# Optimization experiments

Measured on AMD Instinct MI355X. Metric: run time of the kernel, lower is better.

The kernel has to match this reference:

```python
import jax, jax.numpy as jnp
import numpy as np

# Mex config (matches init_kwargs)
B, C, H, W = 64, 64, 64, 64
BLK = (64, 3, 3)        # block over (C, H, W); spans all channels -> out_c = 1
STR = (64, 2, 2)
PAD = (0, 1, 1)
NI = 256                # num_instances
EPS = 1.0
SOFTMAX_MODE = False    # False -> mean (logsumexp - log k), True -> plain logsumexp


def setup_inputs() -> dict:
    key = jax.random.key(0)
    k1, k2 = jax.random.split(key)
    x = jax.random.normal(k1, (B, C, H, W), dtype=jnp.float32)
    kblk = BLK[0] * BLK[1] * BLK[2]
    # Dirichlet([1]*k) init == normalized exponentials; nregions = 1 (shared offsets)
    e = jax.random.exponential(k2, (1, NI, kblk), dtype=jnp.float32)
    offsets = (e / jnp.sum(e, axis=-1, keepdims=True)).reshape(1, NI, *BLK)
    return {"x": x, "offsets": offsets}


def _mex_forward(x, offsets):
    eps = jnp.float32(EPS)
    bc, bh, bw = BLK
    # im2col patch extraction: (B, C*bh*bw, OH, OW); feature dim ordered (c, fh, fw)
    patches = jax.lax.conv_general_dilated_patches(
        x, (bh, bw), (STR[1], STR[2]),
        [(PAD[1], PAD[1]), (PAD[2], PAD[2])],  # zero padding == blocks_out_of_bounds_value
        dimension_numbers=("NCHW", "OIHW", "NCHW"),
    )
    Bn, K, OH, OW = patches.shape  # K = bc*bh*bw = 576
    P = patches.transpose(0, 2, 3, 1).reshape(-1, K)  # (N, k), N = B*OH*OW
    O = offsets.reshape(NI, K)                         # single shared region

    # y_ni = (1/eps) * logsumexp_k( eps*(P_nk + O_ik) ) - log(k)/eps (mean mode)
    # exp-domain GEMM with max-shift for stability:
    Pe = eps * P
    Oe = eps * O
    mp = jnp.max(Pe, axis=1, keepdims=True)   # (N, 1)
    mo = jnp.max(Oe, axis=1, keepdims=True)   # (I, 1)
    S = jnp.exp(Pe - mp) @ jnp.exp(Oe - mo).T  # (N, I)
    y = (jnp.log(S) + mp + mo.T) / eps
    if not SOFTMAX_MODE:
        y = y - jnp.log(jnp.float32(K)) / eps
    # output: (B, num_instances * out_c, OH, OW) with out_c = 1
    return y.reshape(Bn, OH, OW, NI).transpose(0, 3, 1, 2)


def reference(x, offsets):
    return _mex_forward(x, offsets)
```

## Files before the change

### kernel.cpp

```cpp
#include <hip/hip_runtime.h>
#include <hip/hip_bf16.h>


typedef __bf16 bf16x8 __attribute__((ext_vector_type(8)));
typedef float  f32x4  __attribute__((ext_vector_type(4)));

__global__ void mex_prep_b(const float* __restrict__ off, __bf16* __restrict__ Bt) {
    const int i = blockIdx.x * 4 + (threadIdx.x >> 6);
    const int c = threadIdx.x & 63;
    const int c8 = c >> 3, j = c & 7;
    const int wv = i >> 6, nt = (i >> 4) & 3, t16 = i & 15;
    const int q  = c8 & 3;
    const float* oi = off + i * 576;
    #pragma unroll
    for (int p = 0; p < 9; ++p) {
        float v = oi[c * 9 + p];
        const int ks    = p * 2 + (c8 >> 2);
        const int chunk = (ks * 16 + wv * 4 + nt) * 64 + q * 16 + t16;
        Bt[chunk * 8 + j] = (__bf16)__expf(v);
    }
}

__global__ __launch_bounds__(256, 4) void mex_main(
        const float* __restrict__ x,
        const __bf16* __restrict__ Bt,
        float* __restrict__ out) {
    __shared__ bf16x8 lds8[5 * 64 * 8];

    const int bid = blockIdx.x;
    const int b   = bid >> 4;
    const int oh0 = (bid & 15) << 1;
    const int tid  = threadIdx.x;
    const int wv   = tid >> 6;
    const int lane = tid & 63;

    bf16x8 one8;
    #pragma unroll
    for (int j = 0; j < 8; ++j) one8[j] = (__bf16)1.0f;

    if (oh0 == 0) {
        #pragma unroll
        for (int i = 0; i < 2; ++i) lds8[tid + i * 256] = one8;
    }

    {
        const int wp  = tid & 31;
        const int w0  = wp << 1;
        const int c8  = tid >> 5;
        const int c8p = c8 ^ (wp & 7);
        const float* xb = x + ((size_t)b << 18) + w0;
        #pragma unroll
        for (int hl = 0; hl < 5; ++hl) {
            const int hg = 2 * oh0 - 1 + hl;
            if (hg >= 0) {
                const float* xp = xb + (hg << 6);
                float2 v[8];
                #pragma unroll
                for (int k = 0; k < 8; ++k)
                    v[k] = *(const float2*)(xp + (((c8 << 3) + k) << 12));
                bf16x8 ca, cb;
                #pragma unroll
                for (int k = 0; k < 8; ++k) {
                    ca[k] = (__bf16)__expf(v[k].x);
                    cb[k] = (__bf16)__expf(v[k].y);
                }
                bf16x8* dst = lds8 + hl * 512 + w0 * 8 + c8p;
                dst[0] = ca;
                dst[8] = cb;
            }
        }
    }

    const bf16x8* __restrict__ Btv = (const bf16x8*)Bt;
    const int wv4 = wv << 2;
    bf16x8 bcur[4];
    #pragma unroll
    for (int nt = 0; nt < 4; ++nt)
        bcur[nt] = Btv[(wv4 + nt) * 64 + lane];

    __syncthreads();

    const int t16 = tid & 15;
    const int q   = (tid >> 4) & 3;

    int hb[4], wo2[4];
    #pragma unroll
    for (int mt = 0; mt < 4; ++mt) {
        const int m = mt * 16 + t16;
        wo2[mt] = (m & 31) << 1;
        hb[mt]  = (m >> 5) << 7;
    }

    f32x4 acc[4][4];
    #pragma unroll
    for (int mt = 0; mt < 4; ++mt)
        #pragma unroll
        for (int nt = 0; nt < 4; ++nt)
            acc[mt][nt] = (f32x4)(0.0f);

    #pragma unroll
    for (int ks = 0; ks < 18; ++ks) {
        const int p  = ks >> 1;
        const int fh = (p * 11) >> 5;
        const int fw = p - fh * 3;
        const int ccq = ((ks & 1) << 2) + q;

        bf16x8 a[4];
        #pragma unroll
        for (int mt = 0; mt < 4; ++mt) {
            const int wc  = wo2[mt] + fw - 1;
            const int pad = wc < 0;
            const int wcl = pad ? 0 : wc;
            const int row = hb[mt] + fh * 64 + wcl;
            bf16x8 vv = lds8[row * 8 + (ccq ^ ((wcl >> 1) & 7))];
            a[mt] = pad ? one8 : vv;
        }

        bf16x8 bnext[4];
        if (ks < 17) {
            #pragma unroll
            for (int nt = 0; nt < 4; ++nt)
                bnext[nt] = Btv[((ks + 1) * 16 + wv4 + nt) * 64 + lane];
        }

        #pragma unroll
        for (int mt = 0; mt < 4; ++mt)
            #pragma unroll
            for (int nt = 0; nt < 4; ++nt)
                acc[mt][nt] = __builtin_amdgcn_mfma_f32_16x16x32_bf16(
                    a[mt], bcur[nt], acc[mt][nt], 0, 0, 0);

        #pragma unroll
        for (int nt = 0; nt < 4; ++nt) bcur[nt] = bnext[nt];
    }

    const float lK = 6.356107660695891f;
    #pragma unroll
    for (int mt = 0; mt < 4; ++mt) {
        const int m   = mt * 16 + (q << 2);
        const int ohl = m >> 5;
        const int owi = m & 31;
        const int orow = (oh0 + ohl) * 32 + owi;
        #pragma unroll
        for (int nt = 0; nt < 4; ++nt) {
            const int inst = wv * 64 + nt * 16 + t16;
            f32x4 r;
            #pragma unroll
            for (int j = 0; j < 4; ++j)
                r[j] = __logf(acc[mt][nt][j]) - lK;
            *(f32x4*)(out + (((size_t)b * 256 + inst) * 1024 + orow)) = r;
        }
    }
}

extern "C" void kernel_launch(void* const* d_in, const int* in_sizes, int n_in,
                              void* d_out, int out_size, void* d_ws, size_t ws_size,
                              hipStream_t stream) {
    const float* x   = (const float*)d_in[0];
    const float* off = (const float*)d_in[1];
    float* out = (float*)d_out;
    __bf16* Bt = (__bf16*)d_ws;

    mex_prep_b<<<64, 256, 0, stream>>>(off, Bt);
    mex_main<<<1024, 256, 0, stream>>>(x, Bt, out);
}
```

Baseline: 152.1 us.

## Stage output through LDS for coalesced stores and swizzle block order

The epilogue now writes the log-transformed accumulators into shared memory with a padded stride, then rereads them so each thread stores contiguous 128-byte output rows per instance. The old path issued scattered 16-byte stores. The block index is also remapped so that consecutive blocks come from different batches, which changes the order in which workgroups are dispatched across the GPU's partitions. The cost is extra barriers and shared-memory traffic in the epilogue.

```diff
diff --git a/kernel.cpp b/kernel.cpp
--- a/kernel.cpp
+++ b/kernel.cpp
@@ -28,8 +28,9 @@
     __shared__ bf16x8 lds8[5 * 64 * 8];
 
     const int bid = blockIdx.x;
-    const int b   = bid >> 4;
-    const int oh0 = (bid & 15) << 1;
+    const int w   = ((bid & 7) << 7) | (bid >> 3);
+    const int b   = w >> 4;
+    const int oh0 = (w & 15) << 1;
     const int tid  = threadIdx.x;
     const int wv   = tid >> 6;
     const int lane = tid & 63;
@@ -135,21 +136,35 @@
     }
 
     const float lK = 6.356107660695891f;
+    float* lds_f = (float*)lds8;
+    __syncthreads();
     #pragma unroll
-    for (int mt = 0; mt < 4; ++mt) {
-        const int m   = mt * 16 + (q << 2);
-        const int ohl = m >> 5;
-        const int owi = m & 31;
-        const int orow = (oh0 + ohl) * 32 + owi;
+    for (int ohl = 0; ohl < 2; ++ohl) {
         #pragma unroll
-        for (int nt = 0; nt < 4; ++nt) {
-            const int inst = wv * 64 + nt * 16 + t16;
-            f32x4 r;
+        for (int mt2 = 0; mt2 < 2; ++mt2) {
+            const int mt  = ohl * 2 + mt2;
+            const int owi = mt2 * 16 + (q << 2);
             #pragma unroll
-            for (int j = 0; j < 4; ++j)
-                r[j] = __logf(acc[mt][nt][j]) - lK;
-            *(f32x4*)(out + (((size_t)b * 256 + inst) * 1024 + orow)) = r;
+            for (int nt = 0; nt < 4; ++nt) {
+                const int inst = wv * 64 + nt * 16 + t16;
+                f32x4 r;
+                #pragma unroll
+                for (int j = 0; j < 4; ++j)
+                    r[j] = __logf(acc[mt][nt][j]) - lK;
+                *(f32x4*)(lds_f + inst * 36 + owi) = r;
+            }
         }
+        __syncthreads();
+        float* ob = out + ((size_t)b << 18) + ((oh0 + ohl) << 5);
+        #pragma unroll
+        for (int s = 0; s < 8; ++s) {
+            const int g    = tid + s * 256;
+            const int inst = g >> 3;
+            const int owi  = (g & 7) << 2;
+            f32x4 v = *(const f32x4*)(lds_f + inst * 36 + owi);
+            *(f32x4*)(ob + inst * 1024 + owi) = v;
+        }
+        if (ohl == 0) __syncthreads();
     }
 }
 
```

Result: faster. 148.9 us (-2.1%).

## Process two output-row tiles per block with prefetched second tile

Applied to the files above, without the earlier changes.

Each block now handles two consecutive pairs of output rows, launching half as many blocks. While the first tile's MFMA loop runs, the global loads for the second tile are already issued into 40 float2 registers. They are then exponentiated into a second LDS buffer. The block index is also remapped so consecutive blocks cover different batches, which changes L2 locality. This adds heavy register pressure (launch bounds lowered to 2 blocks per SIMD), doubles LDS use, and reduces the block count, which may hurt latency hiding.

```diff
diff --git a/kernel.cpp b/kernel.cpp
--- a/kernel.cpp
+++ b/kernel.cpp
@@ -21,15 +21,18 @@
     }
 }
 
-__global__ __launch_bounds__(256, 4) void mex_main(
+__global__ __launch_bounds__(256, 2) void mex_main(
         const float* __restrict__ x,
         const __bf16* __restrict__ Bt,
         float* __restrict__ out) {
-    __shared__ bf16x8 lds8[5 * 64 * 8];
+    __shared__ bf16x8 lds8[2 * 2560];
 
     const int bid = blockIdx.x;
-    const int b   = bid >> 4;
-    const int oh0 = (bid & 15) << 1;
+    const int wid  = ((bid & 7) << 6) | (bid >> 3);
+    const int b    = wid >> 3;
+    const int j2   = wid & 7;
+    const int oh0a = j2 << 2;
+    const int oh0b = oh0a + 2;
     const int tid  = threadIdx.x;
     const int wv   = tid >> 6;
     const int lane = tid & 63;
@@ -38,37 +41,46 @@
     #pragma unroll
     for (int j = 0; j < 8; ++j) one8[j] = (__bf16)1.0f;
 
-    if (oh0 == 0) {
+    if (oh0a == 0) {
         #pragma unroll
         for (int i = 0; i < 2; ++i) lds8[tid + i * 256] = one8;
     }
 
-    {
-        const int wp  = tid & 31;
-        const int w0  = wp << 1;
-        const int c8  = tid >> 5;
-        const int c8p = c8 ^ (wp & 7);
-        const float* xb = x + ((size_t)b << 18) + w0;
-        #pragma unroll
-        for (int hl = 0; hl < 5; ++hl) {
-            const int hg = 2 * oh0 - 1 + hl;
-            if (hg >= 0) {
-                const float* xp = xb + (hg << 6);
-                float2 v[8];
-                #pragma unroll
-                for (int k = 0; k < 8; ++k)
-                    v[k] = *(const float2*)(xp + (((c8 << 3) + k) << 12));
-                bf16x8 ca, cb;
-                #pragma unroll
-                for (int k = 0; k < 8; ++k) {
-                    ca[k] = (__bf16)__expf(v[k].x);
-                    cb[k] = (__bf16)__expf(v[k].y);
-                }
-                bf16x8* dst = lds8 + hl * 512 + w0 * 8 + c8p;
-                dst[0] = ca;
-                dst[8] = cb;
-            }
-        }
+    const int wp  = tid & 31;
+    const int w0  = wp << 1;
+    const int c8  = tid >> 5;
+    const int c8p = c8 ^ (wp & 7);
+    const float* xb = x + ((size_t)b << 18) + w0;
+
+    #pragma unroll
+    for (int hl = 0; hl < 5; ++hl) {
+        const int hg = 2 * oh0a - 1 + hl;
+        if (hg >= 0) {
+            const float* xp = xb + (hg << 6);
+            float2 v[8];
+            #pragma unroll
+            for (int k = 0; k < 8; ++k)
+                v[k] = *(const float2*)(xp + (((c8 << 3) + k) << 12));
+            bf16x8 ca, cb;
+            #pragma unroll
+            for (int k = 0; k < 8; ++k) {
+                ca[k] = (__bf16)__expf(v[k].x);
+                cb[k] = (__bf16)__expf(v[k].y);
+            }
+            bf16x8* dst = lds8 + hl * 512 + w0 * 8 + c8p;
+            dst[0] = ca;
+            dst[8] = cb;
+        }
+    }
+
+    float2 v1[40];
+    #pragma unroll
+    for (int hl = 0; hl < 5; ++hl) {
+        const int hg = 2 * oh0b - 1 + hl;
+        const float* xp = xb + (hg << 6);
+        #pragma unroll
+        for (int k = 0; k < 8; ++k)
+            v1[hl * 8 + k] = *(const float2*)(xp + (((c8 << 3) + k) << 12));
     }
 
     const bf16x8* __restrict__ Btv = (const bf16x8*)Bt;
@@ -78,11 +90,8 @@
     for (int nt = 0; nt < 4; ++nt)
         bcur[nt] = Btv[(wv4 + nt) * 64 + lane];
 
-    __syncthreads();
-
     const int t16 = tid & 15;
     const int q   = (tid >> 4) & 3;
-
     int hb[4], wo2[4];
     #pragma unroll
     for (int mt = 0; mt < 4; ++mt) {
@@ -90,67 +99,99 @@
         wo2[mt] = (m & 31) << 1;
         hb[mt]  = (m >> 5) << 7;
     }
-
-    f32x4 acc[4][4];
+    const float lK = 6.356107660695891f;
+
+    auto kloop = [&](const bf16x8* __restrict__ L, f32x4 (&acc)[4][4],
+                     bf16x8 (&bc)[4]) {
+        #pragma unroll
+        for (int ks = 0; ks < 18; ++ks) {
+            const int p  = ks >> 1;
+            const int fh = (p * 11) >> 5;
+            const int fw = p - fh * 3;
+            const int ccq = ((ks & 1) << 2) + q;
+            bf16x8 a[4];
+            #pragma unroll
+            for (int mt = 0; mt < 4; ++mt) {
+                const int wc  = wo2[mt] + fw - 1;
+                const int pad = wc < 0;
+                const int wcl = pad ? 0 : wc;
+                const int row = hb[mt] + fh * 64 + wcl;
+                bf16x8 vv = L[row * 8 + (ccq ^ ((wcl >> 1) & 7))];
+                a[mt] = pad ? one8 : vv;
+            }
+            bf16x8 bnext[4];
+            if (ks < 17) {
+                #pragma unroll
+                for (int nt = 0; nt < 4; ++nt)
+                    bnext[nt] = Btv[((ks + 1) * 16 + wv4 + nt) * 64 + lane];
+            }
+            #pragma unroll
+            for (int mt = 0; mt < 4; ++mt)
+                #pragma unroll
+                for (int nt = 0; nt < 4; ++nt)
+                    acc[mt][nt] = __builtin_amdgcn_mfma_f32_16x16x32_bf16(
+                        a[mt], bc[nt], acc[mt][nt], 0, 0, 0);
+            #pragma unroll
+            for (int nt = 0; nt < 4; ++nt) bc[nt] = bnext[nt];
+        }
+    };
+
+    auto epilogue = [&](f32x4 (&acc)[4][4], int oh0) {
+        #pragma unroll
+        for (int mt = 0; mt < 4; ++mt) {
+            const int m   = mt * 16 + (q << 2);
+            const int ohl = m >> 5;
+            const int owi = m & 31;
+            const int orow = (oh0 + ohl) * 32 + owi;
+            #pragma unroll
+            for (int nt = 0; nt < 4; ++nt) {
+                const int inst = wv * 64 + nt * 16 + t16;
+                f32x4 r;
+                #pragma unroll
+                for (int j = 0; j < 4; ++j)
+                    r[j] = __logf(acc[mt][nt][j]) - lK;
+                *(f32x4*)(out + (((size_t)b * 256 + inst) * 1024 + orow)) = r;
+            }
+        }
+    };
+
+    __syncthreads();
+
+    f32x4 acc0[4][4];
     #pragma unroll
     for (int mt = 0; mt < 4; ++mt)
         #pragma unroll
-        for (int nt = 0; nt < 4; ++nt)
-            acc[mt][nt] = (f32x4)(0.0f);
-
-    #pragma unroll
-    for (int ks = 0; ks < 18; ++ks) {
-        const int p  = ks >> 1;
-        const int fh = (p * 11) >> 5;
-        const int fw = p - fh * 3;
-        const int ccq = ((ks & 1) << 2) + q;
-
-        bf16x8 a[4];
-        #pragma unroll
-        for (int mt = 0; mt < 4; ++mt) {
-            const int wc  = wo2[mt] + fw - 1;
-            const int pad = wc < 0;
-            const int wcl = pad ? 0 : wc;
-            const int row = hb[mt] + fh * 64 + wcl;
-            bf16x8 vv = lds8[row * 8 + (ccq ^ ((wcl >> 1) & 7))];
-            a[mt] = pad ? one8 : vv;
-        }
-
-        bf16x8 bnext[4];
-        if (ks < 17) {
-            #pragma unroll
-            for (int nt = 0; nt < 4; ++nt)
-                bnext[nt] = Btv[((ks + 1) * 16 + wv4 + nt) * 64 + lane];
-        }
-
-        #pragma unroll
-        for (int mt = 0; mt < 4; ++mt)
-            #pragma unroll
-            for (int nt = 0; nt < 4; ++nt)
-                acc[mt][nt] = __builtin_amdgcn_mfma_f32_16x16x32_bf16(
-                    a[mt], bcur[nt], acc[mt][nt], 0, 0, 0);
-
-        #pragma unroll
-        for (int nt = 0; nt < 4; ++nt) bcur[nt] = bnext[nt];
-    }
-
-    const float lK = 6.356107660695891f;
-    #pragma unroll
-    for (int mt = 0; mt < 4; ++mt) {
-        const int m   = mt * 16 + (q << 2);
-        const int ohl = m >> 5;
-        const int owi = m & 31;
-        const int orow = (oh0 + ohl) * 32 + owi;
-        #pragma unroll
-        for (int nt = 0; nt < 4; ++nt) {
-            const int inst = wv * 64 + nt * 16 + t16;
-            f32x4 r;
-            #pragma unroll
-            for (int j = 0; j < 4; ++j)
-                r[j] = __logf(acc[mt][nt][j]) - lK;
-            *(f32x4*)(out + (((size_t)b * 256 + inst) * 1024 + orow)) = r;
-        }
-    }
+        for (int nt = 0; nt < 4; ++nt) acc0[mt][nt] = (f32x4)(0.0f);
+    kloop(lds8, acc0, bcur);
+
+    #pragma unroll
+    for (int hl = 0; hl < 5; ++hl) {
+        bf16x8 ca, cb;
+        #pragma unroll
+        for (int k = 0; k < 8; ++k) {
+            ca[k] = (__bf16)__expf(v1[hl * 8 + k].x);
+            cb[k] = (__bf16)__expf(v1[hl * 8 + k].y);
+        }
+        bf16x8* dst = lds8 + 2560 + hl * 512 + w0 * 8 + c8p;
+        dst[0] = ca;
+        dst[8] = cb;
+    }
+    #pragma unroll
+    for (int nt = 0; nt < 4; ++nt)
+        bcur[nt] = Btv[(wv4 + nt) * 64 + lane];
+
+    __syncthreads();
+
+    epilogue(acc0, oh0a);
+
+    f32x4 acc1[4][4];
+    #pragma unroll
+    for (int mt = 0; mt < 4; ++mt)
+        #pragma unroll
+        for (int nt = 0; nt < 4; ++nt) acc1[mt][nt] = (f32x4)(0.0f);
+    kloop(lds8 + 2560, acc1, bcur);
+
+    epilogue(acc1, oh0b);
 }
 
 extern "C" void kernel_launch(void* const* d_in, const int* in_sizes, int n_in,
@@ -162,5 +203,5 @@
     __bf16* Bt = (__bf16*)d_ws;
 
     mex_prep_b<<<64, 256, 0, stream>>>(off, Bt);
-    mex_main<<<1024, 256, 0, stream>>>(x, Bt, out);
+    mex_main<<<512, 256, 0, stream>>>(x, Bt, out);
 }
```

After: 143.8 us. 5.4% less time.

## Process four output-row pairs per block with pipelined halo reuse

Applied to the files above, without the earlier changes.

Each block now covers eight output rows in four stages of two rows, using 512 threads (8 waves of 32 instances each). The next input rows' global loads are issued before the current stage's MFMA loop, and the results are written into per-stage LDS buffers. Each stage reuses the shared halo row from the previous buffer instead of recomputing exp on it. The grid is remapped with an interleaved block order, and the B-operand layout and prefetch now run two k-steps ahead. The aim is to cut redundant halo exp/loads and hide global latency. In exchange it uses larger LDS, fewer blocks (256), and extra barriers.

```diff
diff --git a/kernel.cpp b/kernel.cpp
--- a/kernel.cpp
+++ b/kernel.cpp
@@ -9,27 +9,28 @@
     const int i = blockIdx.x * 4 + (threadIdx.x >> 6);
     const int c = threadIdx.x & 63;
     const int c8 = c >> 3, j = c & 7;
-    const int wv = i >> 6, nt = (i >> 4) & 3, t16 = i & 15;
+    const int g  = i >> 4, t16 = i & 15;
     const int q  = c8 & 3;
     const float* oi = off + i * 576;
     #pragma unroll
     for (int p = 0; p < 9; ++p) {
         float v = oi[c * 9 + p];
         const int ks    = p * 2 + (c8 >> 2);
-        const int chunk = (ks * 16 + wv * 4 + nt) * 64 + q * 16 + t16;
+        const int chunk = (ks * 16 + g) * 64 + q * 16 + t16;
         Bt[chunk * 8 + j] = (__bf16)__expf(v);
     }
 }
 
-__global__ __launch_bounds__(256, 4) void mex_main(
+__global__ __launch_bounds__(512, 2) void mex_main(
         const float* __restrict__ x,
         const __bf16* __restrict__ Bt,
         float* __restrict__ out) {
-    __shared__ bf16x8 lds8[5 * 64 * 8];
+    __shared__ bf16x8 lds8[4 * 2560];
 
     const int bid = blockIdx.x;
-    const int b   = bid >> 4;
-    const int oh0 = (bid & 15) << 1;
+    const int wid = ((bid & 7) << 5) | (bid >> 3);
+    const int b   = wid >> 2;
+    const int ohB = (wid & 3) << 3;
     const int tid  = threadIdx.x;
     const int wv   = tid >> 6;
     const int lane = tid & 63;
@@ -38,20 +39,20 @@
     #pragma unroll
     for (int j = 0; j < 8; ++j) one8[j] = (__bf16)1.0f;
 
-    if (oh0 == 0) {
-        #pragma unroll
-        for (int i = 0; i < 2; ++i) lds8[tid + i * 256] = one8;
-    }
-
-    {
-        const int wp  = tid & 31;
-        const int w0  = wp << 1;
-        const int c8  = tid >> 5;
-        const int c8p = c8 ^ (wp & 7);
-        const float* xb = x + ((size_t)b << 18) + w0;
-        #pragma unroll
-        for (int hl = 0; hl < 5; ++hl) {
-            const int hg = 2 * oh0 - 1 + hl;
+    const int wp   = tid & 31;
+    const int w0   = wp << 1;
+    const int c8   = (tid >> 5) & 7;
+    const int hgrp = tid >> 8;
+    const int c8p  = c8 ^ (wp & 7);
+    const float* xb = x + ((size_t)b << 18) + w0;
+
+    if (ohB == 0) lds8[tid] = one8;
+
+    #pragma unroll
+    for (int rr = 0; rr < 3; ++rr) {
+        const int hl = hgrp * 3 + rr;
+        if (hl < 5) {
+            const int hg = 2 * ohB - 1 + hl;
             if (hg >= 0) {
                 const float* xp = xb + (hg << 6);
                 float2 v[8];
@@ -71,18 +72,45 @@
         }
     }
 
+    float2 va[16], vb[16];
+    auto issue4 = [&](int oh0, float2 (&vv)[16]) {
+        const float* xp = xb + (((oh0 << 1) + (hgrp << 1)) << 6);
+        #pragma unroll
+        for (int rr = 0; rr < 2; ++rr)
+            #pragma unroll
+            for (int k = 0; k < 8; ++k)
+                vv[rr * 8 + k] =
+                    *(const float2*)(xp + (rr << 6) + (((c8 << 3) + k) << 12));
+    };
+    auto write4 = [&](bf16x8* buf, float2 (&vv)[16]) {
+        #pragma unroll
+        for (int rr = 0; rr < 2; ++rr) {
+            const int hl = 1 + (hgrp << 1) + rr;
+            bf16x8 ca, cb;
+            #pragma unroll
+            for (int k = 0; k < 8; ++k) {
+                ca[k] = (__bf16)__expf(vv[rr * 8 + k].x);
+                cb[k] = (__bf16)__expf(vv[rr * 8 + k].y);
+            }
+            bf16x8* dst = buf + hl * 512 + w0 * 8 + c8p;
+            dst[0] = ca;
+            dst[8] = cb;
+        }
+    };
+
     const bf16x8* __restrict__ Btv = (const bf16x8*)Bt;
-    const int wv4 = wv << 2;
-    bf16x8 bcur[4];
-    #pragma unroll
-    for (int nt = 0; nt < 4; ++nt)
-        bcur[nt] = Btv[(wv4 + nt) * 64 + lane];
-
-    __syncthreads();
+    const int g0 = wv << 1;
+    bf16x8 b0[2], b1[2];
+    auto bload = [&]() {
+        #pragma unroll
+        for (int nt = 0; nt < 2; ++nt) {
+            b0[nt] = Btv[(g0 + nt) * 64 + lane];
+            b1[nt] = Btv[(16 + g0 + nt) * 64 + lane];
+        }
+    };
 
     const int t16 = tid & 15;
     const int q   = (tid >> 4) & 3;
-
     int hb[4], wo2[4];
     #pragma unroll
     for (int mt = 0; mt < 4; ++mt) {
@@ -90,67 +118,95 @@
         wo2[mt] = (m & 31) << 1;
         hb[mt]  = (m >> 5) << 7;
     }
-
-    f32x4 acc[4][4];
-    #pragma unroll
-    for (int mt = 0; mt < 4; ++mt)
-        #pragma unroll
-        for (int nt = 0; nt < 4; ++nt)
-            acc[mt][nt] = (f32x4)(0.0f);
-
-    #pragma unroll
-    for (int ks = 0; ks < 18; ++ks) {
-        const int p  = ks >> 1;
-        const int fh = (p * 11) >> 5;
-        const int fw = p - fh * 3;
-        const int ccq = ((ks & 1) << 2) + q;
-
-        bf16x8 a[4];
+    const float lK = 6.356107660695891f;
+
+    auto kloop = [&](const bf16x8* __restrict__ Lc,
+                     const bf16x8* __restrict__ L0, f32x4 (&acc)[4][2]) {
+        #pragma unroll
+        for (int mt = 0; mt < 4; ++mt)
+            #pragma unroll
+            for (int nt = 0; nt < 2; ++nt) acc[mt][nt] = (f32x4)(0.0f);
+        #pragma unroll
+        for (int ks = 0; ks < 18; ++ks) {
+            const int p  = ks >> 1;
+            const int fh = (p * 11) >> 5;
+            const int fw = p - fh * 3;
+            const int ccq = ((ks & 1) << 2) + q;
+            bf16x8 a[4];
+            #pragma unroll
+            for (int mt = 0; mt < 4; ++mt) {
+                const int wc  = wo2[mt] + fw - 1;
+                const int pad = wc < 0;
+                const int wcl = pad ? 0 : wc;
+                const bf16x8* base = (mt < 2 && fh == 0)
+                    ? L0 : (Lc + (hb[mt] + fh * 64) * 8);
+                bf16x8 vv = base[wcl * 8 + (ccq ^ ((wcl >> 1) & 7))];
+                a[mt] = pad ? one8 : vv;
+            }
+            bf16x8 b2[2];
+            if (ks < 16) {
+                #pragma unroll
+                for (int nt = 0; nt < 2; ++nt)
+                    b2[nt] = Btv[((ks + 2) * 16 + g0 + nt) * 64 + lane];
+            }
+            #pragma unroll
+            for (int mt = 0; mt < 4; ++mt)
+                #pragma unroll
+                for (int nt = 0; nt < 2; ++nt)
+                    acc[mt][nt] = __builtin_amdgcn_mfma_f32_16x16x32_bf16(
+                        a[mt], b0[nt], acc[mt][nt], 0, 0, 0);
+            #pragma unroll
+            for (int nt = 0; nt < 2; ++nt) { b0[nt] = b1[nt]; b1[nt] = b2[nt]; }
+        }
+    };
+
+    auto epi = [&](f32x4 (&acc)[4][2], int oh0) {
         #pragma unroll
         for (int mt = 0; mt < 4; ++mt) {
-            const int wc  = wo2[mt] + fw - 1;
-            const int pad = wc < 0;
-            const int wcl = pad ? 0 : wc;
-            const int row = hb[mt] + fh * 64 + wcl;
-            bf16x8 vv = lds8[row * 8 + (ccq ^ ((wcl >> 1) & 7))];
-            a[mt] = pad ? one8 : vv;
-        }
-
-        bf16x8 bnext[4];
-        if (ks < 17) {
-            #pragma unroll
-            for (int nt = 0; nt < 4; ++nt)
-                bnext[nt] = Btv[((ks + 1) * 16 + wv4 + nt) * 64 + lane];
-        }
-
-        #pragma unroll
-        for (int mt = 0; mt < 4; ++mt)
-            #pragma unroll
-            for (int nt = 0; nt < 4; ++nt)
-                acc[mt][nt] = __builtin_amdgcn_mfma_f32_16x16x32_bf16(
-                    a[mt], bcur[nt], acc[mt][nt], 0, 0, 0);
-
-        #pragma unroll
-        for (int nt = 0; nt < 4; ++nt) bcur[nt] = bnext[nt];
-    }
-
-    const float lK = 6.356107660695891f;
-    #pragma unroll
-    for (int mt = 0; mt < 4; ++mt) {
-        const int m   = mt * 16 + (q << 2);
-        const int ohl = m >> 5;
-        const int owi = m & 31;
-        const int orow = (oh0 + ohl) * 32 + owi;
-        #pragma unroll
-        for (int nt = 0; nt < 4; ++nt) {
-            const int inst = wv * 64 + nt * 16 + t16;
-            f32x4 r;
-            #pragma unroll
-            for (int j = 0; j < 4; ++j)
-                r[j] = __logf(acc[mt][nt][j]) - lK;
-            *(f32x4*)(out + (((size_t)b * 256 + inst) * 1024 + orow)) = r;
-        }
-    }
+            const int m   = mt * 16 + (q << 2);
+            const int ohl = m >> 5;
+            const int owi = m & 31;
+            const int orow = (oh0 + ohl) * 32 + owi;
+            #pragma unroll
+            for (int nt = 0; nt < 2; ++nt) {
+                const int inst = wv * 32 + nt * 16 + t16;
+                f32x4 r;
+                #pragma unroll
+                for (int j = 0; j < 4; ++j)
+                    r[j] = __logf(acc[mt][nt][j]) - lK;
+                *(f32x4*)(out + (((size_t)b * 256 + inst) * 1024 + orow)) = r;
+            }
+        }
+    };
+
+    f32x4 accA[4][2], accB[4][2];
+
+    issue4(ohB + 2, va);
+    bload();
+    __syncthreads();
+
+    issue4(ohB + 4, vb);
+    kloop(lds8, lds8, accA);
+    write4(lds8 + 2560, va);
+    bload();
+    __syncthreads();
+
+    issue4(ohB + 6, va);
+    kloop(lds8 + 2560, lds8 + 4 * 512, accB);
+    epi(accA, ohB);
+    write4(lds8 + 2 * 2560, vb);
+    bload();
+    __syncthreads();
+
+    kloop(lds8 + 2 * 2560, lds8 + 2560 + 4 * 512, accA);
+    epi(accB, ohB + 2);
+    write4(lds8 + 3 * 2560, va);
+    bload();
+    __syncthreads();
+
+    kloop(lds8 + 3 * 2560, lds8 + 2 * 2560 + 4 * 512, accB);
+    epi(accA, ohB + 4);
+    epi(accB, ohB + 6);
 }
 
 extern "C" void kernel_launch(void* const* d_in, const int* in_sizes, int n_in,
@@ -162,5 +218,5 @@
     __bf16* Bt = (__bf16*)d_ws;
 
     mex_prep_b<<<64, 256, 0, stream>>>(off, Bt);
-    mex_main<<<1024, 256, 0, stream>>>(x, Bt, out);
+    mex_main<<<256, 512, 0, stream>>>(x, Bt, out);
 }
```

Result: no change. 154.7 us (+1.7%).
